# Optimization experiments

Hardware: AMD Instinct MI355X
Metric: run time of the kernel (lower is better)

Reference implementation:

```python
import jax, jax.numpy as jnp
import numpy as np

B, T, E, H = 4, 2048, 1024, 16
HS = E // H  # head_size = 64


def setup_inputs() -> dict:
    key = jax.random.key(0)
    ks = jax.random.split(key, 5)
    x = jax.random.normal(ks[0], (B, T, E), jnp.float32)
    scale = 0.02
    Wq = jax.random.normal(ks[1], (H, E, HS), jnp.float32) * scale
    Wk = jax.random.normal(ks[2], (H, E, HS), jnp.float32) * scale
    Wv = jax.random.normal(ks[3], (H, E, HS), jnp.float32) * scale
    Wo = jax.random.normal(ks[4], (E, E), jnp.float32) * scale
    bo = jnp.zeros((E,), jnp.float32)
    return {"x": x, "Wq": Wq, "Wk": Wk, "Wv": Wv, "Wo": Wo, "bo": bo}


def reference(x, Wq, Wk, Wv, Wo, bo):
    b, t, e = x.shape
    # per-head projections, batched over heads
    Q = jnp.einsum('bte,hed->bhtd', x, Wq)  # (B,H,T,HS)
    K = jnp.einsum('bte,hed->bhtd', x, Wk)
    V = jnp.einsum('bte,hed->bhtd', x, Wv)
    # faithful quirk 1: scale by sqrt(embd_size), not sqrt(head_size)
    scores = jnp.einsum('bhtd,bhsd->bhts', Q, K) / jnp.sqrt(jnp.float32(e))
    mask = jnp.tril(jnp.ones((t, t), dtype=bool))  # (T_q, T_k)
    scores = jnp.where(mask[None, None, :, :], scores, -jnp.inf)
    # faithful quirk 2: original softmaxes over dim=1 of (B,Tq,Tk) = the QUERY axis
    attn = jax.nn.softmax(scores, axis=2)
    out = jnp.einsum('bhts,bhsd->bhtd', attn, V)  # (B,H,T,HS)
    out = out.transpose(0, 2, 1, 3).reshape(b, t, e)  # concat heads -> (B,T,E)
    return out @ Wo + bo
```

## Files before the change

### kernel.cpp

```cpp
#include <hip/hip_runtime.h>
#include <stdint.h>

#define Bn 4
#define Tn 2048
#define En 1024
#define Hn 16
#define HSn 64
#define BHn (Bn*Hn)
#define NRn (Bn*Tn)

#define CEXP 0.0450840831f

typedef __attribute__((ext_vector_type(8))) short short8;
typedef __attribute__((ext_vector_type(4))) float f32x4;
typedef __attribute__((ext_vector_type(16))) float f32x16;
typedef __attribute__((ext_vector_type(4))) unsigned int uint4w;

__device__ __forceinline__ unsigned short f2b(float f){
  union { float f; unsigned int u; } c; c.f = f;
  unsigned int u = c.u + 0x7FFFu + ((c.u >> 16) & 1u);
  return (unsigned short)(u >> 16);
}
__device__ __forceinline__ float b2f(unsigned short s){
  union { unsigned int u; float f; } c; c.u = ((unsigned int)s) << 16;
  return c.f;
}
__device__ __forceinline__ unsigned int cvtpk(float lo, float hi){
  unsigned int r;
  asm("v_cvt_pk_bf16_f32 %0, %1, %2" : "=v"(r) : "v"(lo), "v"(hi));
  return r;
}
__device__ __forceinline__ f32x4 mfma16(short8 a, short8 b, f32x4 c){
  return __builtin_amdgcn_mfma_f32_16x16x32_bf16(a, b, c, 0, 0, 0);
}
__device__ __forceinline__ f32x16 mfma32(short8 a, short8 b, f32x16 c){
  return __builtin_amdgcn_mfma_f32_32x32x16_bf16(a, b, c, 0, 0, 0);
}
__device__ __forceinline__ void gl16(const void* g, void* s){
  __builtin_amdgcn_global_load_lds((const __attribute__((address_space(1))) unsigned int*)g,
                                   (__attribute__((address_space(3))) unsigned int*)s, 16, 0, 0);
}
#define FENCE()    asm volatile("" ::: "memory")
#define WAITV(N)   asm volatile("s_waitcnt vmcnt(" #N ")" ::: "memory")
#define SBAR()     __builtin_amdgcn_s_barrier()

__global__ void k_cvt_x(const float* __restrict__ x, unsigned short* __restrict__ xb){
  int i = (blockIdx.x * blockDim.x + threadIdx.x) * 8;
  float4 a = *(const float4*)(x + i);
  float4 b = *(const float4*)(x + i + 4);
  alignas(16) unsigned short o[8] = {f2b(a.x),f2b(a.y),f2b(a.z),f2b(a.w),
                                     f2b(b.x),f2b(b.y),f2b(b.z),f2b(b.w)};
  *(uint4w*)(xb + i) = *(const uint4w*)o;
}

__global__ void k_wT(const float* __restrict__ Wq, const float* __restrict__ Wk,
                     const float* __restrict__ Wv, const float* __restrict__ Wo,
                     unsigned short* __restrict__ Wt, unsigned short* __restrict__ Wot)
{
  __shared__ unsigned short Ls[64*80];
  const int tid = threadIdx.x;
  const int ey = blockIdx.x, jt = blockIdx.y;
  const int e0 = ey*64;
  const float* src; int R, c0; unsigned short* outp; float sc = 1.0f;
  if (jt < 48){
    int sel = jt >> 4, h = jt & 15;
    const float* W = (sel==0)?Wq:((sel==1)?Wk:Wv);
    if (sel == 0) sc = CEXP;
    src = W + h*(En*HSn); R = HSn; c0 = 0;
    outp = Wt + jt*64*En;
  } else {
    src = Wo; R = En; c0 = (jt-48)*64;
    outp = Wot + (jt-48)*64*En;
  }
  {
    const int e = tid >> 2, cq = (tid & 3)*16;
    const float* p = src + (e0 + e)*R + c0 + cq;
    float vv[16];
    *(float4*)&vv[0]  = *(const float4*)(p);
    *(float4*)&vv[4]  = *(const float4*)(p+4);
    *(float4*)&vv[8]  = *(const float4*)(p+8);
    *(float4*)&vv[12] = *(const float4*)(p+12);
#pragma unroll
    for (int i = 0; i < 16; i++) Ls[(cq+i)*80 + e] = f2b(vv[i]*sc);
  }
  __syncthreads();
  {
    const int c8 = tid & 7, r = tid >> 3;
#pragma unroll
    for (int rr0 = 0; rr0 < 2; rr0++){
      int rr = r + rr0*32;
      *(uint4w*)(outp + rr*En + e0 + c8*8) = *(const uint4w*)&Ls[rr*80 + c8*8];
    }
  }
}

__global__ void __launch_bounds__(512, 4)
k_qkv(const unsigned short* __restrict__ xb,
      const unsigned short* __restrict__ Wt,
      unsigned short* __restrict__ Qb, unsigned short* __restrict__ Kb,
      unsigned short* __restrict__ Vt)
{
  __shared__ unsigned short As[2][128*64];
  __shared__ unsigned short Bs[2][128*64];
  const int tid = threadIdx.x, lane = tid & 63, w = tid >> 6;
  const int wr = w >> 1, wc = w & 1;
  const int mb = blockIdx.x, nb = blockIdx.y;
  const int n0 = nb*128;
  const int sel = n0 >> 10;
  const int nj0 = n0 & 1023;
  const int l15 = lane & 15, kc = lane >> 4;
  const int r8 = lane >> 3, c7 = lane & 7;
  const int q4 = (lane >> 4)*4;

  const unsigned short* xbase = xb + (mb*128)*En;
  const unsigned short* wbase = Wt + n0*En;

  f32x4 acc[2][4];
#pragma unroll
  for (int i = 0; i < 2; i++)
#pragma unroll
    for (int j = 0; j < 4; j++) acc[i][j] = (f32x4){0.f,0.f,0.f,0.f};

  auto stage = [&](int buf, int k0){
#pragma unroll
    for (int i = 0; i < 2; i++){
      const int rb = w*16 + i*8;
      const int r = rb + r8;
      const int g = (c7 ^ r8) * 8;
      gl16(xbase + r*En + k0 + g, &As[buf][rb*64]);
      gl16(wbase + r*En + k0 + g, &Bs[buf][rb*64]);
    }
  };
  auto compute = [&](int cur){
    const unsigned short* Ac = &As[cur][0];
    const unsigned short* Bc = &Bs[cur][0];
#pragma unroll
    for (int ks = 0; ks < 2; ks++){
      short8 af[2], bf[4];
#pragma unroll
      for (int mf = 0; mf < 2; mf++){
        int ar = wr*32 + mf*16 + l15;
        af[mf] = *(const short8*)&Ac[ar*64 + (((ks*4 + kc) ^ (ar & 7))*8)];
      }
#pragma unroll
      for (int nf = 0; nf < 4; nf++){
        int br = wc*64 + nf*16 + l15;
        bf[nf] = *(const short8*)&Bc[br*64 + (((ks*4 + kc) ^ (br & 7))*8)];
      }
      __builtin_amdgcn_s_setprio(1);
#pragma unroll
      for (int mf = 0; mf < 2; mf++)
#pragma unroll
        for (int nf = 0; nf < 4; nf++)
          acc[mf][nf] = mfma16(af[mf], bf[nf], acc[mf][nf]);
      __builtin_amdgcn_s_setprio(0);
    }
  };

  stage(0, 0);
  stage(1, 64);
  WAITV(4); SBAR();

  for (int kt = 0; kt < 16; kt++){
    const int cur = kt & 1;
    compute(cur);
    FENCE(); SBAR();
    if (kt < 14){
      stage(cur, (kt + 2)*64);
      WAITV(4); SBAR();
    } else if (kt == 14){
      WAITV(0); SBAR();
    }
  }
  __syncthreads();

  const int bb = mb >> 4;
  const int tt0 = (mb*128) & 2047;

  if (sel == 2){
    unsigned short* tb = ((w < 4) ? &As[0][0] + w*2560 : &Bs[0][0] + (w-4)*2560);
#pragma unroll
    for (int nf = 0; nf < 4; nf++)
#pragma unroll
      for (int mf = 0; mf < 2; mf++){
        uint2 u;
        u.x = cvtpk(acc[mf][nf][0], acc[mf][nf][1]);
        u.y = cvtpk(acc[mf][nf][2], acc[mf][nf][3]);
        *(uint2*)&tb[(nf*16 + l15)*40 + mf*16 + q4] = u;
      }
    const int hh = (nj0 >> 6) + wc;
    unsigned short* vb = Vt + ((size_t)(bb*Hn + hh)*HSn)*Tn + tt0 + wr*32;
#pragma unroll
    for (int i = 0; i < 4; i++){
      int rr = i*16 + (lane >> 2);
      int c2 = lane & 3;
      *(uint4w*)(vb + (size_t)rr*Tn + c2*8) = *(const uint4w*)&tb[rr*40 + c2*8];
    }
  } else {
    unsigned short* Out = (sel == 1) ? Kb : Qb;
#pragma unroll
    for (int nf = 0; nf < 4; nf++){
      int jj = nj0 + wc*64 + nf*16 + l15;
      int hh = jj >> 6, dd = jj & 63;
#pragma unroll
      for (int mf = 0; mf < 2; mf++){
#pragma unroll
        for (int q = 0; q < 4; q++){
          int tt = tt0 + wr*32 + mf*16 + q4 + q;
          Out[((bb*Hn + hh)*Tn + tt)*HSn + dd] = f2b(acc[mf][nf][q]);
        }
      }
    }
  }
}

__global__ void __launch_bounds__(256, 3)
k_colsum(const unsigned short* __restrict__ Qb,
         const unsigned short* __restrict__ Kb,
         unsigned short* __restrict__ Vt,
         float* __restrict__ Linv)
{
  __shared__ unsigned short Qs[3][128*64];
  __shared__ float Lred[64];
  const int bh = blockIdx.x*8 + (blockIdx.y & 7);
  const int sb = blockIdx.y >> 3;
  const int s0 = sb * 64;
  const int tid = threadIdx.x, lane = tid & 63, w = tid >> 6;
  const int l5 = lane >> 5, l31 = lane & 31;
  const int r8 = lane >> 3, c7 = lane & 7;

  short8 kf[2][4];
#pragma unroll
  for (int sf = 0; sf < 2; sf++){
    const unsigned short* kr = Kb + (bh*Tn + s0 + sf*32 + l31)*HSn + 8*l5;
#pragma unroll
    for (int ks = 0; ks < 4; ks++) kf[sf][ks] = *(const short8*)(kr + 16*ks);
  }

  float ls[2][16];
#pragma unroll
  for (int sf = 0; sf < 2; sf++)
#pragma unroll
    for (int r = 0; r < 16; r++) ls[sf][r] = 0.f;

  if (tid < 64) Lred[tid] = 0.f;

  const int t0s = (s0 >> 7) << 7;
  const int ntl = (Tn - t0s) >> 7;

  auto stageQ = [&](int buf, int tg0){
#pragma unroll
    for (int i = 0; i < 4; i++){
      int row = (w*4 + i)*8 + r8;
      gl16(Qb + (bh*Tn + tg0 + row)*HSn + ((c7 ^ (row & 7))*8), &Qs[buf][(w*4 + i)*512]);
    }
  };

  stageQ(0, t0s + (ntl-1)*128);
  if (ntl > 1) stageQ(1, t0s + (ntl-2)*128);

  for (int j = 0; j < ntl; j++){
    if (j + 1 < ntl){ WAITV(4); } else { WAITV(0); }
    FENCE(); SBAR(); FENCE();
    if (j + 2 < ntl) stageQ((j + 2) % 3, t0s + (ntl-3-j)*128);

    const int cur = j % 3;
    const int t0 = t0s + (ntl-1-j)*128;
    const int tw = t0 + 32*w;
    if (tw + 31 >= s0){
      f32x16 st[2];
#pragma unroll
      for (int sf = 0; sf < 2; sf++)
#pragma unroll
        for (int r = 0; r < 16; r++) st[sf][r] = 0.f;
      const int qrow = w*32 + l31;
      const unsigned short* Qc = &Qs[cur][qrow*64];
      const int sw = qrow & 7;
      __builtin_amdgcn_s_setprio(1);
#pragma unroll
      for (int ks = 0; ks < 4; ks++){
        short8 qb = *(const short8*)&Qc[((l5 + 2*ks) ^ sw)*8];
        st[0] = mfma32(kf[0][ks], qb, st[0]);
        st[1] = mfma32(kf[1][ks], qb, st[1]);
      }
      __builtin_amdgcn_s_setprio(0);
      const int tg = tw + l31;
      if (s0 + 63 <= tw){
#pragma unroll
        for (int sf = 0; sf < 2; sf++)
#pragma unroll
          for (int r = 0; r < 16; r++)
            ls[sf][r] += __builtin_amdgcn_exp2f(st[sf][r]);
      } else {
#pragma unroll
        for (int sf = 0; sf < 2; sf++)
#pragma unroll
          for (int r = 0; r < 16; r++){
            int sg = s0 + 32*sf + (r & 3) + 8*(r >> 2) + 4*l5;
            float e = __builtin_amdgcn_exp2f(st[sf][r]);
            ls[sf][r] += (tg >= sg) ? e : 0.f;
          }
      }
    }
  }

#pragma unroll
  for (int sf = 0; sf < 2; sf++)
#pragma unroll
    for (int r = 0; r < 16; r++){
      float v = ls[sf][r];
      v += __shfl_xor(v, 1);  v += __shfl_xor(v, 2);
      v += __shfl_xor(v, 4);  v += __shfl_xor(v, 8);
      v += __shfl_xor(v, 16);
      ls[sf][r] = v;
    }
  if (l31 == 0){
#pragma unroll
    for (int sf = 0; sf < 2; sf++)
#pragma unroll
      for (int r = 0; r < 16; r++){
        int sl = 32*sf + (r & 3) + 8*(r >> 2) + 4*l5;
        atomicAdd(&Lred[sl], ls[sf][r]);
      }
  }
  __syncthreads();
  if (tid < 64) Linv[bh*Tn + s0 + tid] = 1.0f / Lred[tid];

  {
    const int d = tid >> 2, cq = (tid & 3)*16;
    unsigned short* vp = Vt + ((size_t)(bh*HSn + d))*Tn + s0 + cq;
    short8 v0 = *(const short8*)vp;
    short8 v1 = *(const short8*)(vp + 8);
    float inv[16];
#pragma unroll
    for (int j = 0; j < 16; j++) inv[j] = 1.0f / Lred[cq + j];
    uint4w o0, o1;
    o0[0] = cvtpk(b2f((unsigned short)v0[0])*inv[0],  b2f((unsigned short)v0[1])*inv[1]);
    o0[1] = cvtpk(b2f((unsigned short)v0[2])*inv[2],  b2f((unsigned short)v0[3])*inv[3]);
    o0[2] = cvtpk(b2f((unsigned short)v0[4])*inv[4],  b2f((unsigned short)v0[5])*inv[5]);
    o0[3] = cvtpk(b2f((unsigned short)v0[6])*inv[6],  b2f((unsigned short)v0[7])*inv[7]);
    o1[0] = cvtpk(b2f((unsigned short)v1[0])*inv[8],  b2f((unsigned short)v1[1])*inv[9]);
    o1[1] = cvtpk(b2f((unsigned short)v1[2])*inv[10], b2f((unsigned short)v1[3])*inv[11]);
    o1[2] = cvtpk(b2f((unsigned short)v1[4])*inv[12], b2f((unsigned short)v1[5])*inv[13]);
    o1[3] = cvtpk(b2f((unsigned short)v1[6])*inv[14], b2f((unsigned short)v1[7])*inv[15]);
    *(uint4w*)vp       = o0;
    *(uint4w*)(vp + 8) = o1;
  }
}

__global__ void __launch_bounds__(256, 3)
k_attn(const unsigned short* __restrict__ Qb,
       const unsigned short* __restrict__ Kb,
       const unsigned short* __restrict__ Vlt,
       unsigned short* __restrict__ Att)
{
  __shared__ unsigned short Ks[3][64*64];
  __shared__ unsigned short Vs[3][64*64];
  const int bh = blockIdx.x*8 + (blockIdx.y & 7);
  const int tb = 15 - (blockIdx.y >> 3);
  const int t0 = tb * 128;
  const int tid = threadIdx.x, lane = tid & 63, w = tid >> 6;
  const int l5 = lane >> 5, l31 = lane & 31;
  const int c7 = lane & 7, r8 = lane >> 3;
  const int tbase = t0 + w*32;
  const int nt = 2*tb + 2;

  short8 qf[4];
  {
    const unsigned short* qr = Qb + (bh*Tn + tbase + l31)*HSn + 8*l5;
#pragma unroll
    for (int ks = 0; ks < 4; ks++) qf[ks] = *(const short8*)(qr + 16*ks);
  }

  f32x16 oacc[2];
#pragma unroll
  for (int df = 0; df < 2; df++)
#pragma unroll
    for (int r = 0; r < 16; r++) oacc[df][r] = 0.f;

  auto stageKV = [&](int buf, int sn){
#pragma unroll
    for (int i = 0; i < 2; i++){
      int row = (w*2 + i)*8 + r8;
      gl16(Kb  + (bh*Tn + sn + row)*HSn + ((c7 ^ (row & 7))*8), &Ks[buf][(w*2 + i)*512]);
      gl16(Vlt + ((size_t)(bh*HSn + row))*Tn + sn + ((c7 ^ (row & 7))*8), &Vs[buf][(w*2 + i)*512]);
    }
  };

  stageKV(0, 0);
  if (nt > 1) stageKV(1, 64);

  for (int it = 0; it < nt; it++){
    if (it + 1 < nt){ WAITV(4); } else { WAITV(0); }
    FENCE(); SBAR(); FENCE();
    if (it + 2 < nt) stageKV((it + 2) % 3, (it + 2)*64);

    const int cur = it % 3;
    const int s0 = it * 64;
    if (s0 <= tbase + 31){
      const unsigned short* Kc = &Ks[cur][0];
      f32x16 st[2];
#pragma unroll
      for (int sf = 0; sf < 2; sf++)
#pragma unroll
        for (int r = 0; r < 16; r++) st[sf][r] = 0.f;
      __builtin_amdgcn_s_setprio(1);
#pragma unroll
      for (int ks = 0; ks < 4; ks++){
#pragma unroll
        for (int sf = 0; sf < 2; sf++){
          int row = sf*32 + l31;
          short8 ka = *(const short8*)&Kc[row*64 + (((l5 + 2*ks) ^ (row & 7))*8)];
          st[sf] = mfma32(ka, qf[ks], st[sf]);
        }
      }
      __builtin_amdgcn_s_setprio(0);

      const int tg = tbase + l31;
      const bool interior = (s0 + 63 <= tbase);
#pragma unroll
      for (int sf = 0; sf < 2; sf++){
#pragma unroll
        for (int r = 0; r < 16; r++){
          float e = __builtin_amdgcn_exp2f(st[sf][r]);
          if (!interior){
            int sg = s0 + 32*sf + (r & 3) + 8*(r >> 2) + 4*l5;
            e = (tg >= sg) ? e : 0.f;
          }
          st[sf][r] = e;
        }
      }

      short8 pb[4];
#pragma unroll
      for (int sf = 0; sf < 2; sf++){
#pragma unroll
        for (int q = 0; q < 2; q++){
          unsigned int ax = cvtpk(st[sf][8*q+0], st[sf][8*q+1]);
          unsigned int ay = cvtpk(st[sf][8*q+2], st[sf][8*q+3]);
          unsigned int bx = cvtpk(st[sf][8*q+4], st[sf][8*q+5]);
          unsigned int by = cvtpk(st[sf][8*q+6], st[sf][8*q+7]);
          asm("v_permlane32_swap_b32 %0, %1" : "+v"(ax), "+v"(bx));
          asm("v_permlane32_swap_b32 %0, %1" : "+v"(ay), "+v"(by));
          union { unsigned int u[4]; short8 s; } pk;
          pk.u[0] = ax; pk.u[1] = ay; pk.u[2] = bx; pk.u[3] = by;
          pb[sf*2 + q] = pk.s;
        }
      }

      const unsigned short* Vc = &Vs[cur][0];
      __builtin_amdgcn_s_setprio(1);
#pragma unroll
      for (int ks = 0; ks < 4; ks++){
#pragma unroll
        for (int df = 0; df < 2; df++){
          int row = df*32 + l31;
          short8 va = *(const short8*)&Vc[row*64 + (((l5 + 2*ks) ^ (row & 7))*8)];
          oacc[df] = mfma32(va, pb[ks], oacc[df]);
        }
      }
      __builtin_amdgcn_s_setprio(0);
    }
  }

  {
    const int tg = tbase + l31;
    unsigned short* ob = Att + (bh*Tn + tg)*HSn;
#pragma unroll
    for (int df = 0; df < 2; df++)
#pragma unroll
      for (int r2 = 0; r2 < 4; r2++){
        uint2 u;
        u.x = cvtpk(oacc[df][r2*4+0], oacc[df][r2*4+1]);
        u.y = cvtpk(oacc[df][r2*4+2], oacc[df][r2*4+3]);
        *(uint2*)&ob[32*df + 8*r2 + 4*l5] = u;
      }
  }
}

__global__ void __launch_bounds__(512, 4)
k_oproj(const unsigned short* __restrict__ Att,
        const unsigned short* __restrict__ Wot,
        const float* __restrict__ bo, float* __restrict__ out)
{
  __shared__ unsigned short As[2][128*64];
  __shared__ unsigned short Bs[2][128*64];
  const int tid = threadIdx.x, lane = tid & 63, w = tid >> 6;
  const int wr = w >> 1, wc = w & 1;
  const int mb = blockIdx.x, nb = blockIdx.y;
  const int n0 = nb*128;
  const int l15 = lane & 15, kc = lane >> 4;
  const int r8 = lane >> 3, c7 = lane & 7;
  const int q4 = (lane >> 4)*4;
  const int bb = mb >> 4;
  const int t0 = (mb*128) & 2047;

  f32x4 acc[2][4];
#pragma unroll
  for (int i = 0; i < 2; i++)
#pragma unroll
    for (int j = 0; j < 4; j++) acc[i][j] = (f32x4){0.f,0.f,0.f,0.f};

  const unsigned short* wbase = Wot + n0*En;

  auto stage = [&](int buf, int k0){
    const int hh = k0 >> 6;
    const unsigned short* abase = Att + ((bb*Hn + hh)*Tn + t0)*HSn;
#pragma unroll
    for (int i = 0; i < 2; i++){
      const int rb = w*16 + i*8;
      const int r = rb + r8;
      const int g = (c7 ^ r8) * 8;
      gl16(abase + r*HSn + g, &As[buf][rb*64]);
      gl16(wbase + r*En + k0 + g, &Bs[buf][rb*64]);
    }
  };
  auto compute = [&](int cur){
    const unsigned short* Ac = &As[cur][0];
    const unsigned short* Bc = &Bs[cur][0];
#pragma unroll
    for (int ks = 0; ks < 2; ks++){
      short8 af[2], bf[4];
#pragma unroll
      for (int mf = 0; mf < 2; mf++){
        int ar = wr*32 + mf*16 + l15;
        af[mf] = *(const short8*)&Ac[ar*64 + (((ks*4 + kc) ^ (ar & 7))*8)];
      }
#pragma unroll
      for (int nf = 0; nf < 4; nf++){
        int br = wc*64 + nf*16 + l15;
        bf[nf] = *(const short8*)&Bc[br*64 + (((ks*4 + kc) ^ (br & 7))*8)];
      }
      __builtin_amdgcn_s_setprio(1);
#pragma unroll
      for (int mf = 0; mf < 2; mf++)
#pragma unroll
        for (int nf = 0; nf < 4; nf++)
          acc[mf][nf] = mfma16(af[mf], bf[nf], acc[mf][nf]);
      __builtin_amdgcn_s_setprio(0);
    }
  };

  stage(0, 0);
  stage(1, 64);
  WAITV(4); SBAR();

  for (int kt = 0; kt < 16; kt++){
    const int cur = kt & 1;
    compute(cur);
    FENCE(); SBAR();
    if (kt < 14){
      stage(cur, (kt + 2)*64);
      WAITV(4); SBAR();
    } else if (kt == 14){
      WAITV(0); SBAR();
    }
  }

#pragma unroll
  for (int nf = 0; nf < 4; nf++){
    int j = n0 + wc*64 + nf*16 + l15;
    float bias = bo[j];
#pragma unroll
    for (int mf = 0; mf < 2; mf++){
#pragma unroll
      for (int q = 0; q < 4; q++){
        int rr = mb*128 + wr*32 + mf*16 + q4 + q;
        out[rr*En + j] = acc[mf][nf][q] + bias;
      }
    }
  }
}

extern "C" void kernel_launch(void* const* d_in, const int* in_sizes, int n_in,
                              void* d_out, int out_size, void* d_ws, size_t ws_size,
                              hipStream_t stream)
{
  (void)in_sizes; (void)n_in; (void)out_size; (void)ws_size;
  const float* x  = (const float*)d_in[0];
  const float* Wq = (const float*)d_in[1];
  const float* Wk = (const float*)d_in[2];
  const float* Wv = (const float*)d_in[3];
  const float* Wo = (const float*)d_in[4];
  const float* bo = (const float*)d_in[5];
  float* out = (float*)d_out;

  uint8_t* w = (uint8_t*)d_ws;
  unsigned short* Qb  = (unsigned short*)(w);
  unsigned short* Kb  = (unsigned short*)(w + (16u << 20));
  unsigned short* Vt  = (unsigned short*)(w + (32u << 20));
  unsigned short* xb  = (unsigned short*)(w + (48u << 20));
  unsigned short* Att = (unsigned short*)(w + (48u << 20));
  unsigned short* Wt  = (unsigned short*)(w + (64u << 20));
  unsigned short* Wot = (unsigned short*)(w + (70u << 20));
  float* Linv         = (float*)(w + (72u << 20));

  hipLaunchKernelGGL(k_cvt_x,  dim3(4096),    dim3(256), 0, stream, x, xb);
  hipLaunchKernelGGL(k_wT,     dim3(16, 64),  dim3(256), 0, stream, Wq, Wk, Wv, Wo, Wt, Wot);
  hipLaunchKernelGGL(k_qkv,    dim3(64, 24),  dim3(512), 0, stream, xb, Wt, Qb, Kb, Vt);
  hipLaunchKernelGGL(k_colsum, dim3(8, 256),  dim3(256), 0, stream, Qb, Kb, Vt, Linv);
  hipLaunchKernelGGL(k_attn,   dim3(8, 128),  dim3(256), 0, stream, Qb, Kb, Vt, Att);
  hipLaunchKernelGGL(k_oproj,  dim3(64, 8),   dim3(512), 0, stream, Att, Wot, bo, out);
}
```

Baseline: 195.5 us.

## Load Q directly to registers in colsum; double-buffer KV in attention

In k_colsum, the triple-buffered LDS staging of Q tiles is replaced by direct per-lane global loads into registers, prefetched one tile ahead. Each warp now exits its loop early once its rows fall entirely below the causal diagonal, and the per-iteration block barrier is removed. In k_attn, K/V staging drops from three LDS buffers to two and reloads the current buffer after a second barrier at the end of each iteration. Occupancy targets rise to 4 and 5 blocks per SM. The cost is uncoalesced-ish register loads of Q, less prefetch distance for K/V, and an extra barrier per iteration.

```diff
diff --git a/kernel.cpp b/kernel.cpp
--- a/kernel.cpp
+++ b/kernel.cpp
@@ -214,20 +214,18 @@
   }
 }
 
-__global__ void __launch_bounds__(256, 3)
+__global__ void __launch_bounds__(256, 4)
 k_colsum(const unsigned short* __restrict__ Qb,
          const unsigned short* __restrict__ Kb,
          unsigned short* __restrict__ Vt,
          float* __restrict__ Linv)
 {
-  __shared__ unsigned short Qs[3][128*64];
   __shared__ float Lred[64];
   const int bh = blockIdx.x*8 + (blockIdx.y & 7);
   const int sb = blockIdx.y >> 3;
   const int s0 = sb * 64;
   const int tid = threadIdx.x, lane = tid & 63, w = tid >> 6;
   const int l5 = lane >> 5, l31 = lane & 31;
-  const int r8 = lane >> 3, c7 = lane & 7;
 
   short8 kf[2][4];
 #pragma unroll
@@ -244,64 +242,54 @@
     for (int r = 0; r < 16; r++) ls[sf][r] = 0.f;
 
   if (tid < 64) Lred[tid] = 0.f;
+  __syncthreads();
 
   const int t0s = (s0 >> 7) << 7;
   const int ntl = (Tn - t0s) >> 7;
-
-  auto stageQ = [&](int buf, int tg0){
-#pragma unroll
-    for (int i = 0; i < 4; i++){
-      int row = (w*4 + i)*8 + r8;
-      gl16(Qb + (bh*Tn + tg0 + row)*HSn + ((c7 ^ (row & 7))*8), &Qs[buf][(w*4 + i)*512]);
-    }
-  };
-
-  stageQ(0, t0s + (ntl-1)*128);
-  if (ntl > 1) stageQ(1, t0s + (ntl-2)*128);
+  const int qrow = w*32 + l31;
+  const unsigned short* qb0 = Qb + ((size_t)bh*Tn + t0s + qrow)*HSn + 8*l5;
+
+  short8 qa[4], qn[4];
+  {
+    const unsigned short* p = qb0 + (size_t)(ntl-1)*128*HSn;
+#pragma unroll
+    for (int ks = 0; ks < 4; ks++) qa[ks] = *(const short8*)(p + 16*ks);
+  }
 
   for (int j = 0; j < ntl; j++){
-    if (j + 1 < ntl){ WAITV(4); } else { WAITV(0); }
-    FENCE(); SBAR(); FENCE();
-    if (j + 2 < ntl) stageQ((j + 2) % 3, t0s + (ntl-3-j)*128);
-
-    const int cur = j % 3;
-    const int t0 = t0s + (ntl-1-j)*128;
-    const int tw = t0 + 32*w;
-    if (tw + 31 >= s0){
-      f32x16 st[2];
-#pragma unroll
-      for (int sf = 0; sf < 2; sf++)
-#pragma unroll
-        for (int r = 0; r < 16; r++) st[sf][r] = 0.f;
-      const int qrow = w*32 + l31;
-      const unsigned short* Qc = &Qs[cur][qrow*64];
-      const int sw = qrow & 7;
+    const int tl = ntl - 1 - j;
+    const int tw = t0s + tl*128 + 32*w;
+    if (tw + 31 < s0) break;
+    if (j + 1 < ntl){
+      const unsigned short* p = qb0 + (size_t)(tl-1)*128*HSn;
+#pragma unroll
+      for (int ks = 0; ks < 4; ks++) qn[ks] = *(const short8*)(p + 16*ks);
+    }
+    const int tg = tw + l31;
+    const bool interior = (s0 + 63 <= tw);
+#pragma unroll
+    for (int sf = 0; sf < 2; sf++){
+      f32x16 st;
+#pragma unroll
+      for (int r = 0; r < 16; r++) st[r] = 0.f;
       __builtin_amdgcn_s_setprio(1);
 #pragma unroll
-      for (int ks = 0; ks < 4; ks++){
-        short8 qb = *(const short8*)&Qc[((l5 + 2*ks) ^ sw)*8];
-        st[0] = mfma32(kf[0][ks], qb, st[0]);
-        st[1] = mfma32(kf[1][ks], qb, st[1]);
-      }
+      for (int ks = 0; ks < 4; ks++) st = mfma32(kf[sf][ks], qa[ks], st);
       __builtin_amdgcn_s_setprio(0);
-      const int tg = tw + l31;
-      if (s0 + 63 <= tw){
-#pragma unroll
-        for (int sf = 0; sf < 2; sf++)
-#pragma unroll
-          for (int r = 0; r < 16; r++)
-            ls[sf][r] += __builtin_amdgcn_exp2f(st[sf][r]);
+      if (interior){
+#pragma unroll
+        for (int r = 0; r < 16; r++) ls[sf][r] += __builtin_amdgcn_exp2f(st[r]);
       } else {
 #pragma unroll
-        for (int sf = 0; sf < 2; sf++)
-#pragma unroll
-          for (int r = 0; r < 16; r++){
-            int sg = s0 + 32*sf + (r & 3) + 8*(r >> 2) + 4*l5;
-            float e = __builtin_amdgcn_exp2f(st[sf][r]);
-            ls[sf][r] += (tg >= sg) ? e : 0.f;
-          }
-      }
-    }
+        for (int r = 0; r < 16; r++){
+          int sg = s0 + 32*sf + (r & 3) + 8*(r >> 2) + 4*l5;
+          float e = __builtin_amdgcn_exp2f(st[r]);
+          ls[sf][r] += (tg >= sg) ? e : 0.f;
+        }
+      }
+    }
+#pragma unroll
+    for (int ks = 0; ks < 4; ks++) qa[ks] = qn[ks];
   }
 
 #pragma unroll
@@ -348,14 +336,14 @@
   }
 }
 
-__global__ void __launch_bounds__(256, 3)
+__global__ void __launch_bounds__(256, 5)
 k_attn(const unsigned short* __restrict__ Qb,
        const unsigned short* __restrict__ Kb,
        const unsigned short* __restrict__ Vlt,
        unsigned short* __restrict__ Att)
 {
-  __shared__ unsigned short Ks[3][64*64];
-  __shared__ unsigned short Vs[3][64*64];
+  __shared__ unsigned short Ks[2][64*64];
+  __shared__ unsigned short Vs[2][64*64];
   const int bh = blockIdx.x*8 + (blockIdx.y & 7);
   const int tb = 15 - (blockIdx.y >> 3);
   const int t0 = tb * 128;
@@ -393,9 +381,8 @@
   for (int it = 0; it < nt; it++){
     if (it + 1 < nt){ WAITV(4); } else { WAITV(0); }
     FENCE(); SBAR(); FENCE();
-    if (it + 2 < nt) stageKV((it + 2) % 3, (it + 2)*64);
-
-    const int cur = it % 3;
+
+    const int cur = it & 1;
     const int s0 = it * 64;
     if (s0 <= tbase + 31){
       const unsigned short* Kc = &Ks[cur][0];
@@ -461,6 +448,9 @@
       }
       __builtin_amdgcn_s_setprio(0);
     }
+
+    FENCE(); SBAR(); FENCE();
+    if (it + 2 < nt) stageKV(cur, (it + 2)*64);
   }
 
   {
```

Result: slower. 255.1 us (+30.5%).
